# Kernel tuning notes

Hardware: AMD Instinct MI355X
Metric: run time of the kernel (lower is better)

The kernel has to match this reference:

```python
import jax, jax.numpy as jnp
import numpy as np

jax.config.update("jax_enable_x64", True)

N = 100000   # active sparse sites
H = W = 512  # event-camera grid
CIN, CMID, COUT = 64, 384, 64
SHIFT = 16   # shift_n


def setup_inputs() -> dict:
    rng = np.random.default_rng(0)
    # unique active coordinates on the grid (batch index 0)
    flat = rng.permutation(H * W)[:N]
    ys, xs = flat // W, flat % W
    # dense index map with 1-pixel halo; sentinel N = missing neighbor
    idx_map = np.full((H + 2, W + 2), N, dtype=np.int32)
    idx_map[ys + 1, xs + 1] = np.arange(N, dtype=np.int32)
    # 3x3 neighborhood indices per active site, row-major kernel order
    nbr = np.stack([idx_map[ys + 1 + dy, xs + 1 + dx]
                    for dy in (-1, 0, 1) for dx in (-1, 0, 1)], axis=1)

    def ri(lo, hi, shape):
        return jnp.asarray(rng.integers(lo, hi, size=shape), dtype=jnp.float32)

    return {
        "feats": ri(-128, 128, (N, CIN)),      # int8-valued input features
        "w1": ri(-128, 128, (CIN, CMID)),       # 1x1 expand weights
        "b1": ri(-1024, 1024, (CMID,)),
        "s1": ri(1, 16, (CMID,)),
        "w_dw": ri(-128, 128, (9, CMID)),       # 3x3 depthwise weights [k, C]
        "b2": ri(-1024, 1024, (CMID,)),
        "s2": ri(1, 64, (CMID,)),
        "w3": ri(-128, 128, (CMID, COUT)),      # 1x1 project weights
        "b3": ri(-1024, 1024, (COUT,)),
        "s3": ri(1, 16, (COUT,)),
        "neighbor_idx": jnp.asarray(nbr),       # [N, 9] int32, N = sentinel
    }


def _quant(psum, bias, scale, relu):
    # (psum + bias) * scale, add 2^(shift-1), arithmetic >> shift,
    # clamp to int8 range, optional relu. psum values are exact integers.
    t = psum.astype(jnp.int64)
    t = ((t + bias.astype(jnp.int64)) * scale.astype(jnp.int64)
         + (1 << (SHIFT - 1))) >> SHIFT
    y = jnp.clip(t.astype(jnp.float32), -128.0, 127.0)
    return jnp.maximum(y, 0.0) if relu else y


def reference(feats, w1, b1, s1, w_dw, b2, s2, w3, b3, s3, neighbor_idx):
    # 1x1 expand (sparse 1x1 conv == matmul over active sites) + quant + relu
    x1 = _quant(feats @ w1, b1, s1, True)                       # [N, CMID]
    # 3x3 depthwise sparse conv: gather 9 neighbors (zero row for missing)
    pad = jnp.concatenate([x1, jnp.zeros((1, x1.shape[1]), x1.dtype)], axis=0)
    psum2 = jnp.einsum('nkc,kc->nc', pad[neighbor_idx], w_dw)   # [N, CMID]
    x2 = _quant(psum2, b2, s2, True)
    # 1x1 project + quant (linear bottleneck: no relu)
    x3 = _quant(x2 @ w3, b3, s3, False)                          # [N, COUT]
    return x3
```

## Files before the change

### kernel.cpp

```cpp
#include <hip/hip_runtime.h>
#include <stdint.h>

#define N_SITES 100000
#define NPAD    100032
#define CIN 64
#define CMID 384
#define COUT 64
#define SHIFT 16

#define FEAT_BLOCKS 6250

typedef int   v4i __attribute__((ext_vector_type(4)));
typedef unsigned int v4u __attribute__((ext_vector_type(4)));
typedef float v4f __attribute__((ext_vector_type(4)));

__global__ __launch_bounds__(256) void pack_all(
    const float* __restrict__ feats,
    const float* __restrict__ w1, const float* __restrict__ w3,
    const float* __restrict__ b1, const float* __restrict__ s1,
    const float* __restrict__ b2, const float* __restrict__ s2,
    const float* __restrict__ b3, const float* __restrict__ s3,
    const float* __restrict__ wdw,
    int8_t* __restrict__ feats8,
    int8_t* __restrict__ w1p, int8_t* __restrict__ w3p,
    int* __restrict__ q1, int* __restrict__ q3,
    int8_t* __restrict__ wdw8, int* __restrict__ bs2,
    int8_t* __restrict__ x1s)
{
    if (blockIdx.x < FEAT_BLOCKS) {
        int i = blockIdx.x * 256 + threadIdx.x;
        if (i >= N_SITES * CIN / 4) return;
        const float4 v = ((const float4*)feats)[i];
        uint32_t w = (uint32_t)(uint8_t)(int8_t)__float2int_rn(v.x)
                   | ((uint32_t)(uint8_t)(int8_t)__float2int_rn(v.y) << 8)
                   | ((uint32_t)(uint8_t)(int8_t)__float2int_rn(v.z) << 16)
                   | ((uint32_t)(uint8_t)(int8_t)__float2int_rn(v.w) << 24);
        ((uint32_t*)feats8)[i] = w;
        return;
    }
    int o = (blockIdx.x - FEAT_BLOCKS) * 256 + threadIdx.x;
    if (o < 24 * 64 * 16) {
        int t = o >> 10, l = (o >> 4) & 63, b = o & 15;
        int k = ((l >> 4) << 4) + b;
        int col = t * 16 + (l & 15);
        w1p[o] = (int8_t)__float2int_rn(w1[k * CMID + col]);
    }
    int o3 = o - 24 * 64 * 16;
    if (o3 >= 0 && o3 < 6 * 4 * 64 * 16) {
        int ks = o3 >> 12, t = (o3 >> 10) & 3;
        int l = (o3 >> 4) & 63, b = o3 & 15;
        int k = ks * 64 + ((l >> 4) << 4) + b;
        int col = t * 16 + (l & 15);
        w3p[o3] = (int8_t)__float2int_rn(w3[k * COUT + col]);
    }
    if (o < 9 * CMID)
        wdw8[o] = (int8_t)__float2int_rn(wdw[o]);
    if (o < CMID) {
        q1[o] = __float2int_rn(b1[o]);
        q1[CMID + o] = __float2int_rn(s1[o]);
        int bb = __float2int_rn(b2[o]);
        int ss = __float2int_rn(s2[o]);
        bs2[o] = (bb & 0xFFFF) | (ss << 16);
        x1s[(size_t)N_SITES * CMID + o] = 0;
    }
    if (o < COUT) {
        q3[o] = __float2int_rn(b3[o]);
        q3[COUT + o] = __float2int_rn(s3[o]);
    }
}

__global__ __launch_bounds__(256) void k1_mfma(
    const int8_t* __restrict__ feats8, const int8_t* __restrict__ w1p,
    const int* __restrict__ q1, int8_t* __restrict__ x1s)
{
    const int lane = threadIdx.x & 63;
    const int wave = threadIdx.x >> 6;
    const int site = blockIdx.x * 64 + wave * 16 + (lane & 15);
    const bool ok = site < N_SITES;
    const int cb = (lane >> 4) << 2;

    const v4i b = *(const v4i*)(feats8 + (size_t)site * CIN + ((lane >> 4) << 4));
    const v4i* ap = (const v4i*)w1p + lane;
    int8_t* orow = x1s + (size_t)site * CMID;
#pragma unroll
    for (int t = 0; t < 24; ++t) {
        v4i a = ap[t * 64];
        v4i acc = {0, 0, 0, 0};
        acc = __builtin_amdgcn_mfma_i32_16x16x64_i8(a, b, acc, 0, 0, 0);
        const int co = t * 16 + cb;
        const v4i bi = *(const v4i*)(q1 + co);
        const v4i si = *(const v4i*)(q1 + CMID + co);
        uint32_t wrd = 0;
#pragma unroll
        for (int r = 0; r < 4; ++r) {
            int v = ((acc[r] + bi[r]) * si[r] + (1 << (SHIFT - 1))) >> SHIFT;
            v = max(0, min(127, v));
            wrd |= (uint32_t)v << (8 * r);
        }
        if (ok) *(uint32_t*)(orow + co) = wrd;
    }
}

__global__ __launch_bounds__(256) void k2_dw(
    const int8_t* __restrict__ x1s, const int* __restrict__ nbr,
    const int8_t* __restrict__ wdw8, const int* __restrict__ bs2,
    int8_t* __restrict__ x2s)
{
    const int g = blockIdx.x * 256 + threadIdx.x;
    const int site = g / 24;
    const int c0 = (g - site * 24) << 4;

    const int* nb = &nbr[site * 9];
    int idx[9];
#pragma unroll
    for (int k = 0; k < 9; ++k) idx[k] = nb[k];

    v4u V[9];
#pragma unroll
    for (int k = 0; k < 9; ++k) {
        const int off = (idx[k] << 8) + (idx[k] << 7) + c0;
        V[k] = *(const v4u*)(x1s + off);
    }

    int acc[16];
#pragma unroll
    for (int j = 0; j < 16; ++j) acc[j] = 0;

#pragma unroll
    for (int k = 0; k < 9; ++k) {
        const v4u W = *(const v4u*)(wdw8 + k * CMID + c0);
#pragma unroll
        for (int j = 0; j < 4; ++j) {
#pragma unroll
            for (int b = 0; b < 4; ++b) {
                const int v = (int)(uint8_t)(V[k][j] >> (8 * b));
                const int w = (int)(int8_t)(W[j] >> (8 * b));
                acc[j * 4 + b] += v * w;
            }
        }
    }

    const v4i BS0 = *(const v4i*)(bs2 + c0);
    const v4i BS1 = *(const v4i*)(bs2 + c0 + 4);
    const v4i BS2 = *(const v4i*)(bs2 + c0 + 8);
    const v4i BS3 = *(const v4i*)(bs2 + c0 + 12);
    const v4i BS[4] = {BS0, BS1, BS2, BS3};

    v4u outw;
#pragma unroll
    for (int j = 0; j < 4; ++j) {
        uint32_t wrd = 0;
#pragma unroll
        for (int b = 0; b < 4; ++b) {
            const int bsv = BS[j][b];
            const int bb = (bsv << 16) >> 16;
            const int ss = bsv >> 16;
            int t = ((acc[j * 4 + b] + bb) * ss + (1 << (SHIFT - 1))) >> SHIFT;
            t = max(0, min(127, t));
            wrd |= (uint32_t)t << (8 * b);
        }
        outw[j] = wrd;
    }
    *(v4u*)(x2s + (site << 8) + (site << 7) + c0) = outw;
}

__global__ __launch_bounds__(256) void k3_mfma(
    const int8_t* __restrict__ x2s, const int8_t* __restrict__ w3p,
    const int* __restrict__ q3, float* __restrict__ out)
{
    const int lane = threadIdx.x & 63;
    const int wave = threadIdx.x >> 6;
    const int site = blockIdx.x * 64 + wave * 16 + (lane & 15);
    const int cb = (lane >> 4) << 2;
    const int8_t* xrow = x2s + (size_t)site * CMID + ((lane >> 4) << 4);

    v4i acc[4] = {{0,0,0,0},{0,0,0,0},{0,0,0,0},{0,0,0,0}};
#pragma unroll
    for (int ks = 0; ks < 6; ++ks) {
        const v4i bfr = *(const v4i*)(xrow + ks * 64);
#pragma unroll
        for (int t = 0; t < 4; ++t) {
            const v4i afr = *((const v4i*)w3p + (ks * 4 + t) * 64 + lane);
            acc[t] = __builtin_amdgcn_mfma_i32_16x16x64_i8(afr, bfr, acc[t], 0, 0, 0);
        }
    }
    if (site < N_SITES) {
        float* orow = out + (size_t)site * COUT;
#pragma unroll
        for (int t = 0; t < 4; ++t) {
            const int co = t * 16 + cb;
            const v4i bo = *(const v4i*)(q3 + co);
            const v4i so = *(const v4i*)(q3 + COUT + co);
            v4f o;
#pragma unroll
            for (int r = 0; r < 4; ++r) {
                int v = ((acc[t][r] + bo[r]) * so[r] + (1 << (SHIFT - 1))) >> SHIFT;
                v = max(-128, min(127, v));
                o[r] = (float)v;
            }
            *(v4f*)(orow + co) = o;
        }
    }
}

extern "C" void kernel_launch(void* const* d_in, const int* in_sizes, int n_in,
                              void* d_out, int out_size, void* d_ws, size_t ws_size,
                              hipStream_t stream) {
    const float* feats = (const float*)d_in[0];
    const float* w1    = (const float*)d_in[1];
    const float* b1    = (const float*)d_in[2];
    const float* s1    = (const float*)d_in[3];
    const float* wdw   = (const float*)d_in[4];
    const float* b2    = (const float*)d_in[5];
    const float* s2    = (const float*)d_in[6];
    const float* w3    = (const float*)d_in[7];
    const float* b3    = (const float*)d_in[8];
    const float* s3    = (const float*)d_in[9];
    const int*   nbr   = (const int*)d_in[10];
    float* out = (float*)d_out;

    int8_t* x1s    = (int8_t*)d_ws;
    int8_t* x2s    = x1s + (size_t)NPAD * CMID;
    int8_t* feats8 = x2s;
    int8_t* w1p    = x2s + (size_t)NPAD * CMID;
    int8_t* w3p    = w1p + 24 * 64 * 16;
    int*    q1     = (int*)(w3p + 6 * 4 * 64 * 16);
    int*    q3     = q1 + 2 * CMID;
    int8_t* wdw8   = (int8_t*)(q3 + 2 * COUT);
    int*    bs2    = (int*)(wdw8 + 9 * CMID);

    pack_all<<<FEAT_BLOCKS + 192, 256, 0, stream>>>(
        feats, w1, w3, b1, s1, b2, s2, b3, s3, wdw,
        feats8, w1p, w3p, q1, q3, wdw8, bs2, x1s);
    k1_mfma<<<NPAD / 64, 256, 0, stream>>>(feats8, w1p, q1, x1s);
    k2_dw<<<N_SITES * 24 / 256, 256, 0, stream>>>(x1s, nbr, wdw8, bs2, x2s);
    k3_mfma<<<NPAD / 64, 256, 0, stream>>>(x2s, w3p, q3, out);
}
```

Baseline: 100.2 us.

## Fuse feature int8 packing into expand kernel and widen depthwise weights

Feature float-to-int8 conversion moves out of the separate pack pass and into the expand MFMA kernel, which now reads fp32 features directly. This removes one full-size read-write pass over the features and leaves a small weight-only pack launch. The depthwise kernel now keeps weights and quant parameters as pre-widened int32 arrays and uses mul24, avoiding byte unpacking and sign extraction. The cost is wider weight loads per thread, and the expand kernel reads four times more bytes per feature row.

```diff
diff --git a/kernel.cpp b/kernel.cpp
--- a/kernel.cpp
+++ b/kernel.cpp
@@ -8,37 +8,22 @@
 #define COUT 64
 #define SHIFT 16
 
-#define FEAT_BLOCKS 6250
-
 typedef int   v4i __attribute__((ext_vector_type(4)));
 typedef unsigned int v4u __attribute__((ext_vector_type(4)));
 typedef float v4f __attribute__((ext_vector_type(4)));
 
-__global__ __launch_bounds__(256) void pack_all(
-    const float* __restrict__ feats,
+__global__ __launch_bounds__(256) void pack_w(
     const float* __restrict__ w1, const float* __restrict__ w3,
     const float* __restrict__ b1, const float* __restrict__ s1,
     const float* __restrict__ b2, const float* __restrict__ s2,
     const float* __restrict__ b3, const float* __restrict__ s3,
     const float* __restrict__ wdw,
-    int8_t* __restrict__ feats8,
     int8_t* __restrict__ w1p, int8_t* __restrict__ w3p,
     int* __restrict__ q1, int* __restrict__ q3,
-    int8_t* __restrict__ wdw8, int* __restrict__ bs2,
+    int* __restrict__ wdw32, int* __restrict__ q2b, int* __restrict__ q2s,
     int8_t* __restrict__ x1s)
 {
-    if (blockIdx.x < FEAT_BLOCKS) {
-        int i = blockIdx.x * 256 + threadIdx.x;
-        if (i >= N_SITES * CIN / 4) return;
-        const float4 v = ((const float4*)feats)[i];
-        uint32_t w = (uint32_t)(uint8_t)(int8_t)__float2int_rn(v.x)
-                   | ((uint32_t)(uint8_t)(int8_t)__float2int_rn(v.y) << 8)
-                   | ((uint32_t)(uint8_t)(int8_t)__float2int_rn(v.z) << 16)
-                   | ((uint32_t)(uint8_t)(int8_t)__float2int_rn(v.w) << 24);
-        ((uint32_t*)feats8)[i] = w;
-        return;
-    }
-    int o = (blockIdx.x - FEAT_BLOCKS) * 256 + threadIdx.x;
+    int o = blockIdx.x * 256 + threadIdx.x;
     if (o < 24 * 64 * 16) {
         int t = o >> 10, l = (o >> 4) & 63, b = o & 15;
         int k = ((l >> 4) << 4) + b;
@@ -54,13 +39,12 @@
         w3p[o3] = (int8_t)__float2int_rn(w3[k * COUT + col]);
     }
     if (o < 9 * CMID)
-        wdw8[o] = (int8_t)__float2int_rn(wdw[o]);
+        wdw32[o] = __float2int_rn(wdw[o]);
     if (o < CMID) {
         q1[o] = __float2int_rn(b1[o]);
         q1[CMID + o] = __float2int_rn(s1[o]);
-        int bb = __float2int_rn(b2[o]);
-        int ss = __float2int_rn(s2[o]);
-        bs2[o] = (bb & 0xFFFF) | (ss << 16);
+        q2b[o] = __float2int_rn(b2[o]);
+        q2s[o] = __float2int_rn(s2[o]);
         x1s[(size_t)N_SITES * CMID + o] = 0;
     }
     if (o < COUT) {
@@ -70,18 +54,30 @@
 }
 
 __global__ __launch_bounds__(256) void k1_mfma(
-    const int8_t* __restrict__ feats8, const int8_t* __restrict__ w1p,
+    const float* __restrict__ feats, const int8_t* __restrict__ w1p,
     const int* __restrict__ q1, int8_t* __restrict__ x1s)
 {
     const int lane = threadIdx.x & 63;
     const int wave = threadIdx.x >> 6;
     const int site = blockIdx.x * 64 + wave * 16 + (lane & 15);
+    const int rsite = min(site, N_SITES - 1);
     const bool ok = site < N_SITES;
     const int cb = (lane >> 4) << 2;
 
-    const v4i b = *(const v4i*)(feats8 + (size_t)site * CIN + ((lane >> 4) << 4));
+    v4i b;
+    const float* fp = feats + (size_t)rsite * CIN + ((lane >> 4) << 4);
+#pragma unroll
+    for (int j = 0; j < 4; ++j) {
+        const v4f f = *(const v4f*)(fp + 4 * j);
+        uint32_t pk = (uint32_t)(__float2int_rn(f[0]) & 255)
+                    | ((uint32_t)(__float2int_rn(f[1]) & 255) << 8)
+                    | ((uint32_t)(__float2int_rn(f[2]) & 255) << 16)
+                    | ((uint32_t)__float2int_rn(f[3]) << 24);
+        b[j] = (int)pk;
+    }
+
     const v4i* ap = (const v4i*)w1p + lane;
-    int8_t* orow = x1s + (size_t)site * CMID;
+    int8_t* orow = x1s + (size_t)rsite * CMID;
 #pragma unroll
     for (int t = 0; t < 24; ++t) {
         v4i a = ap[t * 64];
@@ -103,8 +99,8 @@
 
 __global__ __launch_bounds__(256) void k2_dw(
     const int8_t* __restrict__ x1s, const int* __restrict__ nbr,
-    const int8_t* __restrict__ wdw8, const int* __restrict__ bs2,
-    int8_t* __restrict__ x2s)
+    const int* __restrict__ wdw32, const int* __restrict__ q2b,
+    const int* __restrict__ q2s, int8_t* __restrict__ x2s)
 {
     const int g = blockIdx.x * 256 + threadIdx.x;
     const int site = g / 24;
@@ -128,34 +124,30 @@
 
 #pragma unroll
     for (int k = 0; k < 9; ++k) {
-        const v4u W = *(const v4u*)(wdw8 + k * CMID + c0);
+        v4i W[4];
+#pragma unroll
+        for (int j = 0; j < 4; ++j)
+            W[j] = *(const v4i*)(wdw32 + k * CMID + c0 + 4 * j);
 #pragma unroll
         for (int j = 0; j < 4; ++j) {
 #pragma unroll
             for (int b = 0; b < 4; ++b) {
                 const int v = (int)(uint8_t)(V[k][j] >> (8 * b));
-                const int w = (int)(int8_t)(W[j] >> (8 * b));
-                acc[j * 4 + b] += v * w;
+                acc[j * 4 + b] = __mul24(v, W[j][b]) + acc[j * 4 + b];
             }
         }
     }
 
-    const v4i BS0 = *(const v4i*)(bs2 + c0);
-    const v4i BS1 = *(const v4i*)(bs2 + c0 + 4);
-    const v4i BS2 = *(const v4i*)(bs2 + c0 + 8);
-    const v4i BS3 = *(const v4i*)(bs2 + c0 + 12);
-    const v4i BS[4] = {BS0, BS1, BS2, BS3};
-
     v4u outw;
 #pragma unroll
     for (int j = 0; j < 4; ++j) {
+        const v4i bb = *(const v4i*)(q2b + c0 + 4 * j);
+        const v4i ss = *(const v4i*)(q2s + c0 + 4 * j);
         uint32_t wrd = 0;
 #pragma unroll
         for (int b = 0; b < 4; ++b) {
-            const int bsv = BS[j][b];
-            const int bb = (bsv << 16) >> 16;
-            const int ss = bsv >> 16;
-            int t = ((acc[j * 4 + b] + bb) * ss + (1 << (SHIFT - 1))) >> SHIFT;
+            int t = (__mul24(acc[j * 4 + b] + bb[b], ss[b])
+                     + (1 << (SHIFT - 1))) >> SHIFT;
             t = max(0, min(127, t));
             wrd |= (uint32_t)t << (8 * b);
         }
@@ -219,20 +211,19 @@
     const int*   nbr   = (const int*)d_in[10];
     float* out = (float*)d_out;
 
-    int8_t* x1s    = (int8_t*)d_ws;
-    int8_t* x2s    = x1s + (size_t)NPAD * CMID;
-    int8_t* feats8 = x2s;
-    int8_t* w1p    = x2s + (size_t)NPAD * CMID;
-    int8_t* w3p    = w1p + 24 * 64 * 16;
-    int*    q1     = (int*)(w3p + 6 * 4 * 64 * 16);
-    int*    q3     = q1 + 2 * CMID;
-    int8_t* wdw8   = (int8_t*)(q3 + 2 * COUT);
-    int*    bs2    = (int*)(wdw8 + 9 * CMID);
-
-    pack_all<<<FEAT_BLOCKS + 192, 256, 0, stream>>>(
-        feats, w1, w3, b1, s1, b2, s2, b3, s3, wdw,
-        feats8, w1p, w3p, q1, q3, wdw8, bs2, x1s);
-    k1_mfma<<<NPAD / 64, 256, 0, stream>>>(feats8, w1p, q1, x1s);
-    k2_dw<<<N_SITES * 24 / 256, 256, 0, stream>>>(x1s, nbr, wdw8, bs2, x2s);
+    int8_t* x1s   = (int8_t*)d_ws;
+    int8_t* x2s   = x1s + (size_t)NPAD * CMID;
+    int8_t* w1p   = x2s + (size_t)NPAD * CMID;
+    int8_t* w3p   = w1p + 24 * 64 * 16;
+    int*    q1    = (int*)(w3p + 6 * 4 * 64 * 16);
+    int*    q3    = q1 + 2 * CMID;
+    int*    wdw32 = q3 + 2 * COUT;
+    int*    q2b   = wdw32 + 9 * CMID;
+    int*    q2s   = q2b + CMID;
+
+    pack_w<<<192, 256, 0, stream>>>(w1, w3, b1, s1, b2, s2, b3, s3, wdw,
+                                    w1p, w3p, q1, q3, wdw32, q2b, q2s, x1s);
+    k1_mfma<<<NPAD / 64, 256, 0, stream>>>(feats, w1p, q1, x1s);
+    k2_dw<<<N_SITES * 24 / 256, 256, 0, stream>>>(x1s, nbr, wdw32, q2b, q2s, x2s);
     k3_mfma<<<NPAD / 64, 256, 0, stream>>>(x2s, w3p, q3, out);
 }
```

Measured after the change: 169.1 us. +68.8%, slower.
